# Optimization experiments

Measured on AMD Instinct MI355X. Metric: run time of the kernel, lower is better.

The kernel has to match this reference:

```python
import jax, jax.numpy as jnp
import numpy as np
import math

B, S, E, H, F, L, V = 4, 256, 512, 8, 2048, 4, 32000
HD = E // H
MAXLEN = 5000  # EnhancedPositionalEncoding max_len default


def _ln(x, s, b):
    m = jnp.mean(x, axis=-1, keepdims=True)
    v = jnp.mean((x - m) ** 2, axis=-1, keepdims=True)
    return (x - m) / jnp.sqrt(v + 1e-5) * s + b


def setup_inputs() -> dict:
    key = jax.random.key(0)
    ks = jax.random.split(key, 10)
    n = lambda k, shape: jax.random.normal(k, shape, jnp.float32) * 0.02
    return {
        "src": jax.random.randint(ks[0], (B, S), 0, V),
        "emb": jax.random.uniform(ks[1], (V, E), jnp.float32, -0.1, 0.1),
        "rel_table": n(ks[2], (2 * MAXLEN - 1, E)),
        "norm_in_s": jnp.ones(E, jnp.float32), "norm_in_b": jnp.zeros(E, jnp.float32),
        "inW": n(ks[3], (L, 3 * E, E)), "inB": jnp.zeros((L, 3 * E), jnp.float32),
        "outW": n(ks[4], (L, E, E)), "outB": jnp.zeros((L, E), jnp.float32),
        "ln1_s": jnp.ones((L, E), jnp.float32), "ln1_b": jnp.zeros((L, E), jnp.float32),
        "ln2_s": jnp.ones((L, E), jnp.float32), "ln2_b": jnp.zeros((L, E), jnp.float32),
        "w1": n(ks[5], (L, F, E)), "b1": jnp.zeros((L, F), jnp.float32),
        "w2": n(ks[6], (L, E, F)), "b2": jnp.zeros((L, E), jnp.float32),
        "normf_s": jnp.ones(E, jnp.float32), "normf_b": jnp.zeros(E, jnp.float32),
        "dec_w": jax.random.uniform(ks[7], (V, E), jnp.float32, -0.1, 0.1),
        "dec_b": jnp.zeros(V, jnp.float32),
    }


def reference(src, emb, rel_table, norm_in_s, norm_in_b, inW, inB, outW, outB,
              ln1_s, ln1_b, ln2_s, ln2_b, w1, b1, w2, b2, normf_s, normf_b,
              dec_w, dec_b):
    x = emb[src] * math.sqrt(E)                 # [B,S,E], pos_encoder is identity in relative mode
    x = _ln(x, norm_in_s, norm_in_b)
    # relative-position embedding gather: idx[l,m] = (m - l) + S - 1
    pos = jnp.arange(S)
    rel_idx = (pos[None, :] - pos[:, None]) + S - 1
    rel = rel_table[rel_idx].reshape(S, S, H, HD)  # [S,S,H,hd]
    # NOTE: torch adds the BOOL triu mask to float scores -> +1.0 at masked positions
    mask = jnp.triu(jnp.ones((S, S), jnp.float32), 1)
    scale = 1.0 / math.sqrt(HD)
    for l in range(L):
        h = _ln(x, ln1_s[l], ln1_b[l])
        qkv = h @ inW[l].T + inB[l]
        q, k, v = jnp.split(qkv, 3, axis=-1)
        q = q.reshape(B, S, H, HD).transpose(0, 2, 1, 3)  # [B,H,S,hd]
        k = k.reshape(B, S, H, HD).transpose(0, 2, 1, 3)
        v = v.reshape(B, S, H, HD).transpose(0, 2, 1, 3)
        scores = jnp.einsum('bhqd,bhkd->bhqk', q, k) * scale
        bias = jnp.einsum('bhld,lmhd->bhlm', q, rel)      # relative-position bias (unscaled, as in torch)
        attn = jax.nn.softmax(scores + bias + mask, axis=-1)
        o = jnp.einsum('bhqk,bhkd->bhqd', attn, v).transpose(0, 2, 1, 3).reshape(B, S, E)
        x = x + (o @ outW[l].T + outB[l])
        h2 = _ln(x, ln2_s[l], ln2_b[l])
        ff = jax.nn.gelu(h2 @ w1[l].T + b1[l], approximate=False) @ w2[l].T + b2[l]
        x = x + ff
    x = _ln(x, normf_s, normf_b)  # encoder final norm
    return x @ dec_w.T + dec_b    # [B,S,V]
```

## Files before the change

### kernel.cpp

```cpp
#include <hip/hip_runtime.h>
#include <hip/hip_bf16.h>
#include <math.h>

#define BB 4
#define SS 256
#define EE 512
#define HH 8
#define HD 64
#define FFD 2048
#define LL 4
#define VV 32000
#define BS (BB*SS)
#define SQRT_E 22.627416997969522f
#define ATTN_SCALE 0.125f

typedef __bf16 bf16;
typedef __attribute__((ext_vector_type(4))) __bf16 bf16x4;
typedef __attribute__((ext_vector_type(8))) __bf16 bf16x8;
typedef __attribute__((ext_vector_type(4))) float f32x4;

#define GLOBAL_AS __attribute__((address_space(1)))
#define LDS_AS    __attribute__((address_space(3)))

__device__ __forceinline__ void load_lds16(const bf16* g, bf16* l) {
    __builtin_amdgcn_global_load_lds((const GLOBAL_AS unsigned int*)g,
                                     (LDS_AS unsigned int*)l, 16, 0, 0);
}

__global__ void cvt_all(const float* __restrict__ inW, const float* __restrict__ outW,
                        const float* __restrict__ w1, const float* __restrict__ w2,
                        const float* __restrict__ dec, const float* __restrict__ rel,
                        bf16* __restrict__ inWb, bf16* __restrict__ outWb,
                        bf16* __restrict__ w1b, bf16* __restrict__ w2b,
                        bf16* __restrict__ decb, bf16* __restrict__ relb,
                        const int* __restrict__ src, const float* __restrict__ emb,
                        const float* __restrict__ nsc, const float* __restrict__ nbi,
                        float* __restrict__ xout) {
    int b = blockIdx.x;
    int t = threadIdx.x;
    if (b >= 28544) {
        int row = b - 28544;
        const float* r = emb + (size_t)src[row] * EE;
        float v0 = r[t] * SQRT_E, v1 = r[t + 256] * SQRT_E;
        float sum = v0 + v1, sq = v0 * v0 + v1 * v1;
        #pragma unroll
        for (int off = 32; off; off >>= 1) {
            sum += __shfl_xor(sum, off);
            sq  += __shfl_xor(sq, off);
        }
        __shared__ float ssum[4], ssq[4];
        int wid = t >> 6, lane = t & 63;
        if (lane == 0) { ssum[wid] = sum; ssq[wid] = sq; }
        __syncthreads();
        sum = ssum[0] + ssum[1] + ssum[2] + ssum[3];
        sq  = ssq[0] + ssq[1] + ssq[2] + ssq[3];
        float mean = sum * (1.0f / EE);
        float var  = sq * (1.0f / EE) - mean * mean;
        float rstd = rsqrtf(var + 1e-5f);
        xout[(size_t)row * EE + t]       = (v0 - mean) * rstd * nsc[t] + nbi[t];
        xout[(size_t)row * EE + t + 256] = (v1 - mean) * rstd * nsc[t + 256] + nbi[t + 256];
        return;
    }
    const float* s; bf16* d; int base; int n;
    if (b < 3072)       { s = inW;  d = inWb;  base = b;         n = 3145728; }
    else if (b < 4096)  { s = outW; d = outWb; base = b - 3072;  n = 1048576; }
    else if (b < 8192)  { s = w1;   d = w1b;   base = b - 4096;  n = 4194304; }
    else if (b < 12288) { s = w2;   d = w2b;   base = b - 8192;  n = 4194304; }
    else if (b < 28288) { s = dec;  d = decb;  base = b - 12288; n = 16384000; }
    else                { s = rel;  d = relb;  base = b - 28288; n = 261632; }
    int i = (base * 256 + t) * 4;
    if (i < n) {
        float4 v = *(const float4*)(s + i);
        bf16x4 o;
        o[0] = (bf16)v.x; o[1] = (bf16)v.y; o[2] = (bf16)v.z; o[3] = (bf16)v.w;
        *(bf16x4*)(d + i) = o;
    }
}

template <typename OT>
__global__ void ln_kernel(const float* __restrict__ in, const float* __restrict__ sc,
                          const float* __restrict__ bi, OT* __restrict__ out) {
    int row = blockIdx.x;
    int t = threadIdx.x;
    const float* r = in + (size_t)row * EE;
    float v0 = r[t], v1 = r[t + 256];
    float sum = v0 + v1, sq = v0 * v0 + v1 * v1;
    #pragma unroll
    for (int off = 32; off; off >>= 1) {
        sum += __shfl_xor(sum, off);
        sq  += __shfl_xor(sq, off);
    }
    __shared__ float ssum[4], ssq[4];
    int wid = t >> 6, lane = t & 63;
    if (lane == 0) { ssum[wid] = sum; ssq[wid] = sq; }
    __syncthreads();
    sum = ssum[0] + ssum[1] + ssum[2] + ssum[3];
    sq  = ssq[0] + ssq[1] + ssq[2] + ssq[3];
    float mean = sum * (1.0f / EE);
    float var  = sq * (1.0f / EE) - mean * mean;
    float rstd = rsqrtf(var + 1e-5f);
    out[(size_t)row * EE + t]       = (OT)((v0 - mean) * rstd * sc[t] + bi[t]);
    out[(size_t)row * EE + t + 256] = (OT)((v1 - mean) * rstd * sc[t + 256] + bi[t + 256]);
}

__global__ void embed_ln_kernel(const int* __restrict__ src, const float* __restrict__ emb,
                                const float* __restrict__ sc, const float* __restrict__ bi,
                                float* __restrict__ out) {
    int row = blockIdx.x;
    int t = threadIdx.x;
    const float* r = emb + (size_t)src[row] * EE;
    float v0 = r[t] * SQRT_E, v1 = r[t + 256] * SQRT_E;
    float sum = v0 + v1, sq = v0 * v0 + v1 * v1;
    #pragma unroll
    for (int off = 32; off; off >>= 1) {
        sum += __shfl_xor(sum, off);
        sq  += __shfl_xor(sq, off);
    }
    __shared__ float ssum[4], ssq[4];
    int wid = t >> 6, lane = t & 63;
    if (lane == 0) { ssum[wid] = sum; ssq[wid] = sq; }
    __syncthreads();
    sum = ssum[0] + ssum[1] + ssum[2] + ssum[3];
    sq  = ssq[0] + ssq[1] + ssq[2] + ssq[3];
    float mean = sum * (1.0f / EE);
    float var  = sq * (1.0f / EE) - mean * mean;
    float rstd = rsqrtf(var + 1e-5f);
    out[(size_t)row * EE + t]       = (v0 - mean) * rstd * sc[t] + bi[t];
    out[(size_t)row * EE + t + 256] = (v1 - mean) * rstd * sc[t + 256] + bi[t + 256];
}

template <int BM, int BN, int MODE, int OBF16, int WRVT, int SWZ, int SPLITK>
__global__ __launch_bounds__(256) void gemm_bf16(
        const bf16* __restrict__ A, const bf16* __restrict__ W,
        const float* __restrict__ bias, void* __restrict__ Cout,
        const float* __restrict__ res, bf16* __restrict__ vT,
        int M, int N, int K) {
    constexpr int FM = BM / 32, FN = BN / 32;
    __shared__ bf16 Atile[2][BM * 32];
    __shared__ bf16 Btile[2][BN * 32];
    int tid = threadIdx.x;
    int wid = tid >> 6, lane = tid & 63;
    int wm = (wid >> 1) * (BM / 2), wn = (wid & 1) * (BN / 2);
    int bm, bn;
    if (SWZ) {
        int nbm = gridDim.x;
        int linear = blockIdx.y * nbm + blockIdx.x;
        int total = nbm * gridDim.y;
        int chunk = total >> 3;
        int xcd = linear & 7, idx = linear >> 3;
        int g = xcd * chunk + idx;
        bm = (g % nbm) * BM;
        bn = (g / nbm) * BN;
    } else {
        bm = blockIdx.x * BM;
        bn = blockIdx.y * BN;
    }
    int kp = (SPLITK > 1) ? blockIdx.z : 0;
    int kbeg = kp * (K / SPLITK);
    int kend = kbeg + K / SPLITK;

    f32x4 acc[FM][FN];
    #pragma unroll
    for (int i = 0; i < FM; i++)
        #pragma unroll
        for (int j = 0; j < FN; j++)
            acc[i][j] = (f32x4){0.f, 0.f, 0.f, 0.f};

    int mrow = lane & 15, kq = (lane >> 4) * 8;

    auto stage = [&](int buf, int k0) {
        #pragma unroll
        for (int it = 0; it < BM / 64; it++) {
            int c = it * 256 + tid;
            int row = c >> 2, kc = (c & 3) * 8;
            load_lds16(A + (size_t)(bm + row) * K + k0 + kc, &Atile[buf][c * 8]);
        }
        #pragma unroll
        for (int it = 0; it < BN / 64; it++) {
            int c = it * 256 + tid;
            int row = c >> 2, kc = (c & 3) * 8;
            load_lds16(W + (size_t)(bn + row) * K + k0 + kc, &Btile[buf][c * 8]);
        }
    };

    stage(0, kbeg);
    __syncthreads();
    int cur = 0;
    for (int k0 = kbeg; k0 < kend; k0 += 32) {
        if (k0 + 32 < kend) stage(cur ^ 1, k0 + 32);
        bf16x8 af[FM], bfv[FN];
        #pragma unroll
        for (int i = 0; i < FM; i++)
            af[i] = *(const bf16x8*)(&Atile[cur][(wm + i * 16 + mrow) * 32 + kq]);
        #pragma unroll
        for (int j = 0; j < FN; j++)
            bfv[j] = *(const bf16x8*)(&Btile[cur][(wn + j * 16 + mrow) * 32 + kq]);
        #pragma unroll
        for (int i = 0; i < FM; i++)
            #pragma unroll
            for (int j = 0; j < FN; j++)
                acc[i][j] = __builtin_amdgcn_mfma_f32_16x16x32_bf16(af[i], bfv[j], acc[i][j], 0, 0, 0);
        __syncthreads();
        cur ^= 1;
    }

    #pragma unroll
    for (int i = 0; i < FM; i++) {
        int row0 = bm + wm + i * 16 + (lane >> 4) * 4;
        #pragma unroll
        for (int j = 0; j < FN; j++) {
            int col = bn + wn + j * 16 + (lane & 15);
            float bv = bias[col];
            #pragma unroll
            for (int r = 0; r < 4; r++) {
                int row = row0 + r;
                if (SPLITK > 1) {
                    float v = acc[i][j][r];
                    if (kp == 0) v += bv;
                    atomicAdd((float*)Cout + (size_t)row * N + col, v);
                    continue;
                }
                float v = acc[i][j][r] + bv;
                if (MODE == 1) v = 0.5f * v * (1.0f + erff(v * 0.7071067811865476f));
                if (MODE == 2) v += res[(size_t)row * N + col];
                if (WRVT && col >= 1024) {
                    int cc = col - 1024;
                    vT[(size_t)(((row >> 8) * 8 + (cc >> 6)) * 64 + (cc & 63)) * 256 + (row & 255)] = (bf16)v;
                } else if (OBF16) ((bf16*)Cout)[(size_t)row * N + col] = (bf16)v;
                else              ((float*)Cout)[(size_t)row * N + col] = v;
            }
        }
    }
}

__global__ __launch_bounds__(256) void attn_mfma(const bf16* __restrict__ qkv,
        const bf16* __restrict__ relb, const bf16* __restrict__ vT,
        bf16* __restrict__ o) {
    int blk = blockIdx.x;
    int qt = blk & 3, bh = blk >> 2;
    int h = bh & 7, b = bh >> 3;
    int q0 = qt * 64, j0 = 192 - q0;
    int tid = threadIdx.x;
    int wid = tid >> 6, lane = tid & 63;
    int l15 = lane & 15, quad = lane >> 4;
    int mr0 = wid * 16;

    __shared__ __align__(16) bf16 Qs[64 * 72];
    __shared__ __align__(16) bf16 Stg[64 * 72];
    __shared__ __align__(16) bf16 BP[64 * 264];

    int c0 = tid, c1 = 256 + tid;
    int r0 = c0 >> 3, ch0 = (c0 & 7) * 8;
    int r1 = c1 >> 3, ch1 = (c1 & 7) * 8;

    const size_t qbase = (size_t)(b * 256 + q0) * 1536 + h * 64;
    *(bf16x8*)(Qs + r0 * 72 + ch0) = *(const bf16x8*)(qkv + qbase + (size_t)r0 * 1536 + ch0);
    *(bf16x8*)(Qs + r1 * 72 + ch1) = *(const bf16x8*)(qkv + qbase + (size_t)r1 * 1536 + ch1);

    bf16x8 pf0, pf1;
    {
        const size_t rb = (size_t)j0 * 512 + h * 64;
        pf0 = *(const bf16x8*)(relb + rb + (size_t)r0 * 512 + ch0);
        pf1 = *(const bf16x8*)(relb + rb + (size_t)r1 * 512 + ch1);
    }

    __syncthreads();
    bf16x8 af0 = *(const bf16x8*)(Qs + (mr0 + l15) * 72 + quad * 8);
    bf16x8 af1 = *(const bf16x8*)(Qs + (mr0 + l15) * 72 + 32 + quad * 8);

    f32x4 S[16];
    #pragma unroll
    for (int i = 0; i < 16; i++) S[i] = (f32x4){0.f, 0.f, 0.f, 0.f};

    for (int jc = 0; jc < 5; jc++) {
        *(bf16x8*)(Stg + r0 * 72 + ch0) = pf0;
        *(bf16x8*)(Stg + r1 * 72 + ch1) = pf1;
        __syncthreads();
        if (jc < 4) {
            const size_t rb = (size_t)(j0 + (jc + 1) * 64) * 512 + h * 64;
            pf0 = *(const bf16x8*)(relb + rb + (size_t)r0 * 512 + ch0);
            pf1 = *(const bf16x8*)(relb + rb + (size_t)r1 * 512 + ch1);
        } else {
            const size_t kb = (size_t)(b * 256) * 1536 + 512 + h * 64;
            pf0 = *(const bf16x8*)(qkv + kb + (size_t)r0 * 1536 + ch0);
            pf1 = *(const bf16x8*)(qkv + kb + (size_t)r1 * 1536 + ch1);
        }
        #pragma unroll
        for (int jt = 0; jt < 4; jt++) {
            f32x4 acc = (f32x4){0.f, 0.f, 0.f, 0.f};
            bf16x8 bv0 = *(const bf16x8*)(Stg + (jt * 16 + l15) * 72 + quad * 8);
            bf16x8 bv1 = *(const bf16x8*)(Stg + (jt * 16 + l15) * 72 + 32 + quad * 8);
            acc = __builtin_amdgcn_mfma_f32_16x16x32_bf16(af0, bv0, acc, 0, 0, 0);
            acc = __builtin_amdgcn_mfma_f32_16x16x32_bf16(af1, bv1, acc, 0, 0, 0);
            int jp = jc * 64 + jt * 16 + l15;
            #pragma unroll
            for (int r = 0; r < 4; r++) {
                int ll = mr0 + quad * 4 + r;
                int m = jp + ll - 63;
                if (m >= 0 && m < 256) BP[ll * 256 + m] = (bf16)acc[r];
            }
        }
        __syncthreads();
    }

    for (int kc = 0; kc < 4; kc++) {
        *(bf16x8*)(Stg + r0 * 72 + ch0) = pf0;
        *(bf16x8*)(Stg + r1 * 72 + ch1) = pf1;
        __syncthreads();
        if (kc < 3) {
            const size_t kb = (size_t)(b * 256 + (kc + 1) * 64) * 1536 + 512 + h * 64;
            pf0 = *(const bf16x8*)(qkv + kb + (size_t)r0 * 1536 + ch0);
            pf1 = *(const bf16x8*)(qkv + kb + (size_t)r1 * 1536 + ch1);
        } else {
            const size_t vb = (size_t)(bh * 64) * 256;
            pf0 = *(const bf16x8*)(vT + vb + (size_t)r0 * 256 + ch0);
            pf1 = *(const bf16x8*)(vT + vb + (size_t)r1 * 256 + ch1);
        }
        #pragma unroll
        for (int nt = 0; nt < 4; nt++) {
            bf16x8 bv0 = *(const bf16x8*)(Stg + (nt * 16 + l15) * 72 + quad * 8);
            bf16x8 bv1 = *(const bf16x8*)(Stg + (nt * 16 + l15) * 72 + 32 + quad * 8);
            S[kc * 4 + nt] = __builtin_amdgcn_mfma_f32_16x16x32_bf16(af0, bv0, S[kc * 4 + nt], 0, 0, 0);
            S[kc * 4 + nt] = __builtin_amdgcn_mfma_f32_16x16x32_bf16(af1, bv1, S[kc * 4 + nt], 0, 0, 0);
        }
        __syncthreads();
    }

    float rmax[4] = {-1e30f, -1e30f, -1e30f, -1e30f};
    #pragma unroll
    for (int T = 0; T < 16; T++) {
        int m = T * 16 + l15;
        #pragma unroll
        for (int r = 0; r < 4; r++) {
            int ll = mr0 + quad * 4 + r;
            float v = S[T][r] * ATTN_SCALE + (float)BP[ll * 256 + m]
                      + ((m > q0 + ll) ? 1.0f : 0.0f);
            S[T][r] = v;
            rmax[r] = fmaxf(rmax[r], v);
        }
    }
    #pragma unroll
    for (int r = 0; r < 4; r++)
        #pragma unroll
        for (int d = 1; d < 16; d <<= 1)
            rmax[r] = fmaxf(rmax[r], __shfl_xor(rmax[r], d));
    float rsum[4] = {0.f, 0.f, 0.f, 0.f};
    #pragma unroll
    for (int T = 0; T < 16; T++)
        #pragma unroll
        for (int r = 0; r < 4; r++) {
            float p = expf(S[T][r] - rmax[r]);
            S[T][r] = p;
            rsum[r] += p;
        }
    #pragma unroll
    for (int r = 0; r < 4; r++)
        #pragma unroll
        for (int d = 1; d < 16; d <<= 1)
            rsum[r] += __shfl_xor(rsum[r], d);

    __syncthreads();
    #pragma unroll
    for (int T = 0; T < 16; T++)
        #pragma unroll
        for (int r = 0; r < 4; r++)
            BP[(mr0 + quad * 4 + r) * 264 + T * 16 + l15] = (bf16)S[T][r];

    f32x4 oacc[4];
    #pragma unroll
    for (int i = 0; i < 4; i++) oacc[i] = (f32x4){0.f, 0.f, 0.f, 0.f};
    for (int kc = 0; kc < 4; kc++) {
        *(bf16x8*)(Stg + r0 * 72 + ch0) = pf0;
        *(bf16x8*)(Stg + r1 * 72 + ch1) = pf1;
        __syncthreads();
        if (kc < 3) {
            const size_t vb = (size_t)(bh * 64) * 256 + (kc + 1) * 64;
            pf0 = *(const bf16x8*)(vT + vb + (size_t)r0 * 256 + ch0);
            pf1 = *(const bf16x8*)(vT + vb + (size_t)r1 * 256 + ch1);
        }
        #pragma unroll
        for (int ks = 0; ks < 2; ks++) {
            bf16x8 ap = *(const bf16x8*)(BP + (mr0 + l15) * 264 + kc * 64 + ks * 32 + quad * 8);
            #pragma unroll
            for (int nt = 0; nt < 4; nt++) {
                bf16x8 bv = *(const bf16x8*)(Stg + (nt * 16 + l15) * 72 + ks * 32 + quad * 8);
                oacc[nt] = __builtin_amdgcn_mfma_f32_16x16x32_bf16(ap, bv, oacc[nt], 0, 0, 0);
            }
        }
        __syncthreads();
    }

    #pragma unroll
    for (int nt = 0; nt < 4; nt++)
        #pragma unroll
        for (int r = 0; r < 4; r++) {
            int ll = mr0 + quad * 4 + r;
            o[(size_t)(b * 256 + q0 + ll) * 512 + h * 64 + nt * 16 + l15] =
                (bf16)(oacc[nt][r] * (1.0f / rsum[r]));
        }
}

template <int MODE>
__global__ void gemm_nt(const float* __restrict__ A, const float* __restrict__ W,
                        const float* __restrict__ bias, float* __restrict__ C,
                        const float* __restrict__ res, int M, int N, int K) {
    __shared__ float As[64][17];
    __shared__ float Ws[64][17];
    int tid = threadIdx.x;
    int tx = tid & 15, ty = tid >> 4;
    int bm = blockIdx.y * 64, bn = blockIdx.x * 64;
    float acc[4][4] = {};
    for (int k0 = 0; k0 < K; k0 += 16) {
        #pragma unroll
        for (int i = 0; i < 4; i++) {
            int idx = tid + i * 256;
            int r = idx >> 4, c = idx & 15;
            As[r][c] = A[(size_t)(bm + r) * K + k0 + c];
            Ws[r][c] = W[(size_t)(bn + r) * K + k0 + c];
        }
        __syncthreads();
        #pragma unroll
        for (int kk = 0; kk < 16; kk++) {
            float a[4], w[4];
            #pragma unroll
            for (int i = 0; i < 4; i++) a[i] = As[ty * 4 + i][kk];
            #pragma unroll
            for (int j = 0; j < 4; j++) w[j] = Ws[tx * 4 + j][kk];
            #pragma unroll
            for (int i = 0; i < 4; i++)
                #pragma unroll
                for (int j = 0; j < 4; j++)
                    acc[i][j] += a[i] * w[j];
        }
        __syncthreads();
    }
    #pragma unroll
    for (int i = 0; i < 4; i++) {
        int row = bm + ty * 4 + i;
        #pragma unroll
        for (int j = 0; j < 4; j++) {
            int col = bn + tx * 4 + j;
            float v = acc[i][j] + bias[col];
            if (MODE == 1) v = 0.5f * v * (1.0f + erff(v * 0.7071067811865476f));
            if (MODE == 2) v += res[(size_t)row * N + col];
            C[(size_t)row * N + col] = v;
        }
    }
}

__global__ void attn_kernel(const float* __restrict__ qkv, const float* __restrict__ rel_table,
                            float* __restrict__ o) {
    int blk = blockIdx.x;
    int l = blk & (SS - 1);
    int bh = blk >> 8;
    int h = bh & (HH - 1);
    int b = bh >> 3;
    int t = threadIdx.x;
    int wid = t >> 6, lane = t & 63;

    __shared__ float qs[HD];
    __shared__ float attn_s[SS];
    __shared__ float swave[4];
    __shared__ float opart[4][HD];

    const float* qrow = qkv + (size_t)(b * SS + l) * (3 * EE) + h * HD;
    if (t < HD) qs[t] = qrow[t];
    __syncthreads();

    const float* krow   = qkv + (size_t)(b * SS + t) * (3 * EE) + EE + h * HD;
    const float* relrow = rel_table + (size_t)(t - l + SS - 1) * EE + h * HD;
    const float4* k4 = reinterpret_cast<const float4*>(krow);
    const float4* r4 = reinterpret_cast<const float4*>(relrow);
    float s1 = 0.f, s2 = 0.f;
    #pragma unroll
    for (int d4 = 0; d4 < HD / 4; d4++) {
        float4 kv = k4[d4], rv = r4[d4];
        float q0 = qs[4 * d4], q1 = qs[4 * d4 + 1], q2 = qs[4 * d4 + 2], q3 = qs[4 * d4 + 3];
        s1 += q0 * kv.x + q1 * kv.y + q2 * kv.z + q3 * kv.w;
        s2 += q0 * rv.x + q1 * rv.y + q2 * rv.z + q3 * rv.w;
    }
    float val = s1 * ATTN_SCALE + s2 + ((t > l) ? 1.0f : 0.0f);

    float m = val;
    #pragma unroll
    for (int off = 32; off; off >>= 1) m = fmaxf(m, __shfl_xor(m, off));
    if (lane == 0) swave[wid] = m;
    __syncthreads();
    m = fmaxf(fmaxf(swave[0], swave[1]), fmaxf(swave[2], swave[3]));
    float p = expf(val - m);
    float s = p;
    #pragma unroll
    for (int off = 32; off; off >>= 1) s += __shfl_xor(s, off);
    __syncthreads();
    if (lane == 0) swave[wid] = s;
    __syncthreads();
    float tot = swave[0] + swave[1] + swave[2] + swave[3];
    attn_s[t] = p;
    __syncthreads();

    int d = t & 63, part = t >> 6;
    const float* vbase = qkv + (size_t)(b * SS) * (3 * EE) + 2 * EE + h * HD + d;
    float acc = 0.f;
    int m0 = part * 64;
    #pragma unroll 8
    for (int mm = m0; mm < m0 + 64; mm++)
        acc += attn_s[mm] * vbase[(size_t)mm * (3 * EE)];
    opart[part][d] = acc;
    __syncthreads();
    if (t < 64) {
        float ov = (opart[0][d] + opart[1][d] + opart[2][d] + opart[3][d]) / tot;
        o[(size_t)(b * SS + l) * EE + h * HD + d] = ov;
    }
}

extern "C" void kernel_launch(void* const* d_in, const int* in_sizes, int n_in,
                              void* d_out, int out_size, void* d_ws, size_t ws_size,
                              hipStream_t stream) {
    const int*   src    = (const int*)  d_in[0];
    const float* emb    = (const float*)d_in[1];
    const float* rel    = (const float*)d_in[2];
    const float* nin_s  = (const float*)d_in[3];
    const float* nin_b  = (const float*)d_in[4];
    const float* inW    = (const float*)d_in[5];
    const float* inB    = (const float*)d_in[6];
    const float* outW   = (const float*)d_in[7];
    const float* outB   = (const float*)d_in[8];
    const float* ln1_s  = (const float*)d_in[9];
    const float* ln1_b  = (const float*)d_in[10];
    const float* ln2_s  = (const float*)d_in[11];
    const float* ln2_b  = (const float*)d_in[12];
    const float* w1     = (const float*)d_in[13];
    const float* b1     = (const float*)d_in[14];
    const float* w2     = (const float*)d_in[15];
    const float* b2     = (const float*)d_in[16];
    const float* normf_s= (const float*)d_in[17];
    const float* normf_b= (const float*)d_in[18];
    const float* dec_w  = (const float*)d_in[19];
    const float* dec_b  = (const float*)d_in[20];
    float* out = (float*)d_out;

    const size_t n_inW  = (size_t)LL * 3 * EE * EE;
    const size_t n_outW = (size_t)LL * EE * EE;
    const size_t n_w1   = (size_t)LL * FFD * EE;
    const size_t n_w2   = (size_t)LL * EE * FFD;
    const size_t n_dec  = (size_t)VV * EE;

    float* x    = (float*)d_ws;
    bf16*  qkvb = (bf16*)(x + (size_t)BS * EE);
    bf16*  hb   = qkvb + (size_t)BS * 3 * EE;
    bf16*  ob   = hb + (size_t)BS * EE;
    bf16*  ffb  = ob + (size_t)BS * EE;
    bf16*  vTb  = ffb + (size_t)BS * FFD;
    bf16*  relb = vTb + (size_t)BS * 512;
    bf16*  inWb  = relb + (size_t)512 * EE;
    bf16*  outWb = inWb + n_inW;
    bf16*  w1b   = outWb + n_outW;
    bf16*  w2b   = w1b + n_w1;
    bf16*  decWb = w2b + n_w2;
    size_t needed = (size_t)((char*)(decWb + n_dec) - (char*)d_ws);

    if (ws_size >= needed) {
        cvt_all<<<29568, 256, 0, stream>>>(inW, outW, w1, w2, dec_w, rel,
                                           inWb, outWb, w1b, w2b, decWb, relb,
                                           src, emb, nin_s, nin_b, x);

        for (int l = 0; l < LL; l++) {
            ln_kernel<bf16><<<BS, 256, 0, stream>>>(x, ln1_s + l * EE, ln1_b + l * EE, hb);
            gemm_bf16<64, 64, 0, 1, 1, 0, 1><<<dim3(BS / 64, 3 * EE / 64), 256, 0, stream>>>(
                hb, inWb + (size_t)l * 3 * EE * EE, inB + (size_t)l * 3 * EE, qkvb, nullptr,
                vTb, BS, 3 * EE, EE);
            attn_mfma<<<BB * HH * 4, 256, 0, stream>>>(qkvb, relb, vTb, ob);
            gemm_bf16<64, 64, 2, 0, 0, 0, 2><<<dim3(BS / 64, EE / 64, 2), 256, 0, stream>>>(
                ob, outWb + (size_t)l * EE * EE, outB + (size_t)l * EE, x, x,
                nullptr, BS, EE, EE);
            ln_kernel<bf16><<<BS, 256, 0, stream>>>(x, ln2_s + l * EE, ln2_b + l * EE, hb);
            gemm_bf16<64, 64, 1, 1, 0, 0, 1><<<dim3(BS / 64, FFD / 64), 256, 0, stream>>>(
                hb, w1b + (size_t)l * FFD * EE, b1 + (size_t)l * FFD, ffb, nullptr,
                nullptr, BS, FFD, EE);
            gemm_bf16<64, 64, 2, 0, 0, 0, 4><<<dim3(BS / 64, EE / 64, 4), 256, 0, stream>>>(
                ffb, w2b + (size_t)l * EE * FFD, b2 + (size_t)l * EE, x, x,
                nullptr, BS, EE, FFD);
        }

        ln_kernel<bf16><<<BS, 256, 0, stream>>>(x, normf_s, normf_b, hb);
        gemm_bf16<128, 128, 0, 0, 0, 1, 1><<<dim3(BS / 128, VV / 128), 256, 0, stream>>>(
            hb, decWb, dec_b, out, nullptr, nullptr, BS, VV, EE);
    } else {
        float* h     = x + (size_t)BS * EE;
        float* qkvf  = h + (size_t)BS * EE;
        float* o     = qkvf + (size_t)BS * 3 * EE;
        float* ffmid = o + (size_t)BS * EE;

        embed_ln_kernel<<<BS, 256, 0, stream>>>(src, emb, nin_s, nin_b, x);
        for (int l = 0; l < LL; l++) {
            ln_kernel<float><<<BS, 256, 0, stream>>>(x, ln1_s + l * EE, ln1_b + l * EE, h);
            gemm_nt<0><<<dim3(3 * EE / 64, BS / 64), 256, 0, stream>>>(
                h, inW + (size_t)l * 3 * EE * EE, inB + (size_t)l * 3 * EE, qkvf, nullptr,
                BS, 3 * EE, EE);
            attn_kernel<<<BB * HH * SS, 256, 0, stream>>>(qkvf, rel, o);
            gemm_nt<2><<<dim3(EE / 64, BS / 64), 256, 0, stream>>>(
                o, outW + (size_t)l * EE * EE, outB + (size_t)l * EE, x, x,
                BS, EE, EE);
            ln_kernel<float><<<BS, 256, 0, stream>>>(x, ln2_s + l * EE, ln2_b + l * EE, h);
            gemm_nt<1><<<dim3(FFD / 64, BS / 64), 256, 0, stream>>>(
                h, w1 + (size_t)l * FFD * EE, b1 + (size_t)l * FFD, ffmid, nullptr,
                BS, FFD, EE);
            gemm_nt<2><<<dim3(EE / 64, BS / 64), 256, 0, stream>>>(
                ffmid, w2 + (size_t)l * EE * FFD, b2 + (size_t)l * EE, x, x,
                BS, EE, FFD);
        }
        ln_kernel<float><<<BS, 256, 0, stream>>>(x, normf_s, normf_b, h);
        gemm_nt<0><<<dim3(VV / 64, BS / 64), 256, 0, stream>>>(
            h, dec_w, dec_b, out, nullptr, BS, VV, EE);
    }
}
```

Measured before the change: 577.2 us.

## Fuse pre-LayerNorm into QKV and FFN1 GEMMs via LDS-resident A panel

Removes the separate LayerNorm kernels before the QKV and first FFN GEMMs. Each GEMM block now computes LayerNorm for its 64 rows itself and writes the full normalized bf16 A panel (K=512, padded) into LDS, so only the weight tiles are streamed through the loop. It also raises split-K for the out-projection (2 to 4) and the FFN2 GEMM (4 to 8). The cost is that LN work is repeated by every N-block, LDS use per block grows (about 66KB), which may lower occupancy, and more split-K partials are accumulated into x.

Result: slower. 910.6 us (+57.8%).

```diff
diff --git a/kernel.cpp b/kernel.cpp
--- a/kernel.cpp
+++ b/kernel.cpp
@@ -129,18 +129,21 @@
     out[(size_t)row * EE + t + 256] = (v1 - mean) * rstd * sc[t + 256] + bi[t + 256];
 }
 
-template <int BM, int BN, int MODE, int OBF16, int WRVT, int SWZ, int SPLITK>
+template <int BM, int BN, int MODE, int OBF16, int WRVT, int SWZ, int SPLITK, int LNF>
 __global__ __launch_bounds__(256) void gemm_bf16(
-        const bf16* __restrict__ A, const bf16* __restrict__ W,
-        const float* __restrict__ bias, void* __restrict__ Cout,
-        const float* __restrict__ res, bf16* __restrict__ vT,
-        int M, int N, int K) {
+        const bf16* __restrict__ A, const float* __restrict__ Xf,
+        const float* __restrict__ lnsc, const float* __restrict__ lnbi,
+        const bf16* __restrict__ W, const float* __restrict__ bias,
+        void* __restrict__ Cout, const float* __restrict__ res,
+        bf16* __restrict__ vT, int M, int N, int K) {
     constexpr int FM = BM / 32, FN = BN / 32;
-    __shared__ bf16 Atile[2][BM * 32];
-    __shared__ bf16 Btile[2][BN * 32];
+    constexpr int APAD = 520;
+    __shared__ __align__(16) bf16 Asm[LNF ? (BM * APAD) : (2 * BM * 32)];
+    __shared__ __align__(16) bf16 Bsm[2 * BN * 32];
     int tid = threadIdx.x;
     int wid = tid >> 6, lane = tid & 63;
     int wm = (wid >> 1) * (BM / 2), wn = (wid & 1) * (BN / 2);
+    int mrow = lane & 15, kq = (lane >> 4) * 8;
     int bm, bn;
     if (SWZ) {
         int nbm = gridDim.x;
@@ -166,35 +169,80 @@
         for (int j = 0; j < FN; j++)
             acc[i][j] = (f32x4){0.f, 0.f, 0.f, 0.f};
 
-    int mrow = lane & 15, kq = (lane >> 4) * 8;
-
-    auto stage = [&](int buf, int k0) {
+    auto stageA = [&](int buf, int k0) {
         #pragma unroll
         for (int it = 0; it < BM / 64; it++) {
             int c = it * 256 + tid;
             int row = c >> 2, kc = (c & 3) * 8;
-            load_lds16(A + (size_t)(bm + row) * K + k0 + kc, &Atile[buf][c * 8]);
-        }
+            load_lds16(A + (size_t)(bm + row) * K + k0 + kc, Asm + buf * BM * 32 + c * 8);
+        }
+    };
+    auto stageB = [&](int buf, int k0) {
         #pragma unroll
         for (int it = 0; it < BN / 64; it++) {
             int c = it * 256 + tid;
             int row = c >> 2, kc = (c & 3) * 8;
-            load_lds16(W + (size_t)(bn + row) * K + k0 + kc, &Btile[buf][c * 8]);
+            load_lds16(W + (size_t)(bn + row) * K + k0 + kc, Bsm + buf * BN * 32 + c * 8);
         }
     };
 
-    stage(0, kbeg);
+    if (LNF) {
+        stageB(0, kbeg);
+        int row = tid >> 2, sub = tid & 3;
+        const float* xr = Xf + (size_t)(bm + row) * 512 + sub * 128;
+        float sum = 0.f, sq = 0.f;
+        #pragma unroll
+        for (int j = 0; j < 128; j += 4) {
+            float4 v = *(const float4*)(xr + j);
+            sum += v.x + v.y + v.z + v.w;
+            sq  += v.x * v.x + v.y * v.y + v.z * v.z + v.w * v.w;
+        }
+        sum += __shfl_xor(sum, 1); sq += __shfl_xor(sq, 1);
+        sum += __shfl_xor(sum, 2); sq += __shfl_xor(sq, 2);
+        float mean = sum * (1.0f / 512.0f);
+        float var  = sq * (1.0f / 512.0f) - mean * mean;
+        float rstd = rsqrtf(var + 1e-5f);
+        #pragma unroll
+        for (int j = 0; j < 128; j += 8) {
+            float4 a = *(const float4*)(xr + j);
+            float4 b = *(const float4*)(xr + j + 4);
+            const float* sc = lnsc + sub * 128 + j;
+            const float* bi = lnbi + sub * 128 + j;
+            float4 s0 = *(const float4*)sc, s1 = *(const float4*)(sc + 4);
+            float4 b0 = *(const float4*)bi, b1 = *(const float4*)(bi + 4);
+            bf16x8 o;
+            o[0] = (bf16)((a.x - mean) * rstd * s0.x + b0.x);
+            o[1] = (bf16)((a.y - mean) * rstd * s0.y + b0.y);
+            o[2] = (bf16)((a.z - mean) * rstd * s0.z + b0.z);
+            o[3] = (bf16)((a.w - mean) * rstd * s0.w + b0.w);
+            o[4] = (bf16)((b.x - mean) * rstd * s1.x + b1.x);
+            o[5] = (bf16)((b.y - mean) * rstd * s1.y + b1.y);
+            o[6] = (bf16)((b.z - mean) * rstd * s1.z + b1.z);
+            o[7] = (bf16)((b.w - mean) * rstd * s1.w + b1.w);
+            *(bf16x8*)(Asm + row * APAD + sub * 128 + j) = o;
+        }
+    } else {
+        stageA(0, kbeg);
+        stageB(0, kbeg);
+    }
     __syncthreads();
     int cur = 0;
     for (int k0 = kbeg; k0 < kend; k0 += 32) {
-        if (k0 + 32 < kend) stage(cur ^ 1, k0 + 32);
+        if (k0 + 32 < kend) {
+            if (!LNF) stageA(cur ^ 1, k0 + 32);
+            stageB(cur ^ 1, k0 + 32);
+        }
         bf16x8 af[FM], bfv[FN];
         #pragma unroll
-        for (int i = 0; i < FM; i++)
-            af[i] = *(const bf16x8*)(&Atile[cur][(wm + i * 16 + mrow) * 32 + kq]);
+        for (int i = 0; i < FM; i++) {
+            if (LNF)
+                af[i] = *(const bf16x8*)(Asm + (wm + i * 16 + mrow) * APAD + k0 + kq);
+            else
+                af[i] = *(const bf16x8*)(Asm + cur * BM * 32 + (wm + i * 16 + mrow) * 32 + kq);
+        }
         #pragma unroll
         for (int j = 0; j < FN; j++)
-            bfv[j] = *(const bf16x8*)(&Btile[cur][(wn + j * 16 + mrow) * 32 + kq]);
+            bfv[j] = *(const bf16x8*)(Bsm + cur * BN * 32 + (wn + j * 16 + mrow) * 32 + kq);
         #pragma unroll
         for (int i = 0; i < FM; i++)
             #pragma unroll
@@ -565,26 +613,28 @@
                                            src, emb, nin_s, nin_b, x);
 
         for (int l = 0; l < LL; l++) {
-            ln_kernel<bf16><<<BS, 256, 0, stream>>>(x, ln1_s + l * EE, ln1_b + l * EE, hb);
-            gemm_bf16<64, 64, 0, 1, 1, 0, 1><<<dim3(BS / 64, 3 * EE / 64), 256, 0, stream>>>(
-                hb, inWb + (size_t)l * 3 * EE * EE, inB + (size_t)l * 3 * EE, qkvb, nullptr,
-                vTb, BS, 3 * EE, EE);
+            gemm_bf16<64, 64, 0, 1, 1, 0, 1, 1><<<dim3(BS / 64, 3 * EE / 64), 256, 0, stream>>>(
+                nullptr, x, ln1_s + (size_t)l * EE, ln1_b + (size_t)l * EE,
+                inWb + (size_t)l * 3 * EE * EE, inB + (size_t)l * 3 * EE,
+                qkvb, nullptr, vTb, BS, 3 * EE, EE);
             attn_mfma<<<BB * HH * 4, 256, 0, stream>>>(qkvb, relb, vTb, ob);
-            gemm_bf16<64, 64, 2, 0, 0, 0, 2><<<dim3(BS / 64, EE / 64, 2), 256, 0, stream>>>(
-                ob, outWb + (size_t)l * EE * EE, outB + (size_t)l * EE, x, x,
-                nullptr, BS, EE, EE);
-            ln_kernel<bf16><<<BS, 256, 0, stream>>>(x, ln2_s + l * EE, ln2_b + l * EE, hb);
-            gemm_bf16<64, 64, 1, 1, 0, 0, 1><<<dim3(BS / 64, FFD / 64), 256, 0, stream>>>(
-                hb, w1b + (size_t)l * FFD * EE, b1 + (size_t)l * FFD, ffb, nullptr,
-                nullptr, BS, FFD, EE);
-            gemm_bf16<64, 64, 2, 0, 0, 0, 4><<<dim3(BS / 64, EE / 64, 4), 256, 0, stream>>>(
-                ffb, w2b + (size_t)l * EE * FFD, b2 + (size_t)l * EE, x, x,
-                nullptr, BS, EE, FFD);
+            gemm_bf16<64, 64, 2, 0, 0, 0, 4, 0><<<dim3(BS / 64, EE / 64, 4), 256, 0, stream>>>(
+                ob, nullptr, nullptr, nullptr,
+                outWb + (size_t)l * EE * EE, outB + (size_t)l * EE,
+                x, x, nullptr, BS, EE, EE);
+            gemm_bf16<64, 64, 1, 1, 0, 0, 1, 1><<<dim3(BS / 64, FFD / 64), 256, 0, stream>>>(
+                nullptr, x, ln2_s + (size_t)l * EE, ln2_b + (size_t)l * EE,
+                w1b + (size_t)l * FFD * EE, b1 + (size_t)l * FFD,
+                ffb, nullptr, nullptr, BS, FFD, EE);
+            gemm_bf16<64, 64, 2, 0, 0, 0, 8, 0><<<dim3(BS / 64, EE / 64, 8), 256, 0, stream>>>(
+                ffb, nullptr, nullptr, nullptr,
+                w2b + (size_t)l * EE * FFD, b2 + (size_t)l * EE,
+                x, x, nullptr, BS, EE, FFD);
         }
 
         ln_kernel<bf16><<<BS, 256, 0, stream>>>(x, normf_s, normf_b, hb);
-        gemm_bf16<128, 128, 0, 0, 0, 1, 1><<<dim3(BS / 128, VV / 128), 256, 0, stream>>>(
-            hb, decWb, dec_b, out, nullptr, nullptr, BS, VV, EE);
+        gemm_bf16<128, 128, 0, 0, 0, 1, 1, 0><<<dim3(BS / 128, VV / 128), 256, 0, stream>>>(
+            hb, nullptr, nullptr, nullptr, decWb, dec_b, out, nullptr, nullptr, BS, VV, EE);
     } else {
         float* h     = x + (size_t)BS * EE;
         float* qkvf  = h + (size_t)BS * EE;
```
